# Kernel optimization log

Hardware: AMD Instinct MI355X
Metric: run time of the kernel (lower is better)

Reference implementation:

```python
import jax, jax.numpy as jnp
import numpy as np

HIDDEN = 768
HEAD = 64


def setup_inputs() -> dict:
    key = jax.random.key(0)
    ks = jax.random.split(key, 9)
    s = 1.0 / np.sqrt(HIDDEN)
    so = 1.0 / np.sqrt(HEAD)
    return {
        "x": jax.random.normal(ks[0], (4, 4096, HIDDEN), dtype=jnp.float32),
        "Wq": jax.random.uniform(ks[1], (HIDDEN, HEAD), jnp.float32, -s, s),
        "bq": jax.random.uniform(ks[2], (HEAD,), jnp.float32, -s, s),
        "Wk": jax.random.uniform(ks[3], (HIDDEN, HEAD), jnp.float32, -s, s),
        "bk": jax.random.uniform(ks[4], (HEAD,), jnp.float32, -s, s),
        "Wv": jax.random.uniform(ks[5], (HIDDEN, HEAD), jnp.float32, -s, s),
        "bv": jax.random.uniform(ks[6], (HEAD,), jnp.float32, -s, s),
        "Wo": jax.random.uniform(ks[7], (HEAD, HIDDEN), jnp.float32, -so, so),
        "bo": jax.random.uniform(ks[8], (HIDDEN,), jnp.float32, -so, so),
    }


def reference(x, Wq, bq, Wk, bk, Wv, bv, Wo, bo):
    # x: [b, s, h]
    q = jnp.einsum('bsh,hd->bsd', x, Wq) + bq  # [b, s, d]
    k = jnp.einsum('bsh,hd->bsd', x, Wk) + bk
    v = jnp.einsum('bsh,hd->bsd', x, Wv) + bv
    scale = 1.0 / jnp.sqrt(jnp.asarray(HEAD, x.dtype))
    scores = jnp.einsum('bqd,bkd->bqk', q, k) * scale  # [b, s, s]
    A = jax.nn.softmax(scores, axis=-1)
    ctx = jnp.einsum('bqk,bkd->bqd', A, v)  # [b, s, d]
    return jnp.einsum('bsd,dh->bsh', ctx, Wo) + bo
```

## Files before the change

### kernel.cpp

```cpp
#include <hip/hip_runtime.h>
#include <hip/hip_bf16.h>
#include <stdint.h>

#define BB 4
#define SS 4096
#define HH 768
#define DD 64

typedef __attribute__((ext_vector_type(8))) short bf16x8;
typedef __attribute__((ext_vector_type(4))) short bf16x4;
typedef __attribute__((ext_vector_type(4))) float f32x4;
typedef __attribute__((ext_vector_type(2))) float f32x2;
typedef __attribute__((ext_vector_type(16))) float f32x16;
typedef __attribute__((ext_vector_type(4))) uint32_t u32x4;
typedef __attribute__((ext_vector_type(2))) uint32_t u32x2;

typedef const __attribute__((address_space(1))) uint32_t g_u32;
typedef __attribute__((address_space(3))) uint32_t l_u32;
#define ASYNC16(gp, lp) \
  __builtin_amdgcn_global_load_lds((g_u32*)(gp), (l_u32*)(lp), 16, 0, 0)

__device__ __forceinline__ short f2bf(float f) {
  uint32_t u = __builtin_bit_cast(uint32_t, f);
  u += 0x7fffu + ((u >> 16) & 1u);
  return (short)(u >> 16);
}

#define QSCALE 0.18033688011112042f

__global__ __launch_bounds__(256) void prep_kernel(
    const float* __restrict__ Wq, const float* __restrict__ bq,
    const float* __restrict__ Wk, const float* __restrict__ bk,
    const float* __restrict__ Wv, const float* __restrict__ bv,
    const float* __restrict__ Wo,
    short* __restrict__ wqkvF, float* __restrict__ bqkv,
    short* __restrict__ woF) {
  int idx = blockIdx.x * 256 + threadIdx.x;
  const int N1 = 192 * HH;
  const int N2 = HH * DD;
  if (idx < N1) {
    int n = idx / HH, k = idx % HH;
    float v;
    if (n < 64)       v = Wq[k * 64 + n] * QSCALE;
    else if (n < 128) v = Wk[k * 64 + (n - 64)];
    else              v = Wv[k * 64 + (n - 128)];
    int tile = (n >> 4) * 24 + (k >> 5);
    int lane = (((k >> 3) & 3) << 4) | (n & 15);
    wqkvF[tile * 512 + lane * 8 + (k & 7)] = f2bf(v);
  } else if (idx < N1 + N2) {
    int j = idx - N1;
    int n = j / 64, k = j % 64;
    int tile = (n >> 4) * 2 + (k >> 5);
    int lane = (((k >> 3) & 3) << 4) | (n & 15);
    woF[tile * 512 + lane * 8 + (k & 7)] = f2bf(Wo[k * HH + n]);
  } else if (idx < N1 + N2 + 192) {
    int n = idx - N1 - N2;
    float v;
    if (n < 64)       v = bq[n] * QSCALE;
    else if (n < 128) v = bk[n - 64];
    else              v = bv[n - 128];
    bqkv[n] = v;
  }
}

__global__ __launch_bounds__(256, 2) void qkv_kernel(
    const float* __restrict__ x, const short* __restrict__ wF,
    const float* __restrict__ bqkv,
    short* __restrict__ qb, short* __restrict__ kb, short* __restrict__ vT) {
  __shared__ short xl[32 * 776];
  __shared__ short vtile[64 * 32];
  const int tid = threadIdx.x;
  const int w = tid >> 6, lane = tid & 63, g = (lane >> 4) & 3, n16 = lane & 15;
  const int m0 = blockIdx.x * 32;

  const float4* xsrc = (const float4*)&x[m0 * HH];
#pragma unroll
  for (int i = 0; i < 24; ++i) {
    int idx = i * 256 + tid;
    const float4 f = xsrc[idx];
    int elem = idx * 4;
    int row = elem / HH, col = elem % HH;
    bf16x4 p = { f2bf(f.x), f2bf(f.y), f2bf(f.z), f2bf(f.w) };
    *(bf16x4*)&xl[row * 776 + col] = p;
  }
  __syncthreads();

  f32x4 acc[2][3] = {};
  const short* wbase = &wF[w * 36864 + lane * 8];

#pragma unroll 2
  for (int kc = 0; kc < 24; ++kc) {
    const int ko = kc * 32 + g * 8;
    bf16x8 a0 = *(const bf16x8*)&xl[n16 * 776 + ko];
    bf16x8 a1 = *(const bf16x8*)&xl[(16 + n16) * 776 + ko];
    bf16x8 b0 = *(const bf16x8*)&wbase[kc * 512];
    bf16x8 b1 = *(const bf16x8*)&wbase[12288 + kc * 512];
    bf16x8 b2 = *(const bf16x8*)&wbase[24576 + kc * 512];
    acc[0][0] = __builtin_amdgcn_mfma_f32_16x16x32_bf16(a0, b0, acc[0][0], 0, 0, 0);
    acc[1][0] = __builtin_amdgcn_mfma_f32_16x16x32_bf16(a1, b0, acc[1][0], 0, 0, 0);
    acc[0][1] = __builtin_amdgcn_mfma_f32_16x16x32_bf16(a0, b1, acc[0][1], 0, 0, 0);
    acc[1][1] = __builtin_amdgcn_mfma_f32_16x16x32_bf16(a1, b1, acc[1][1], 0, 0, 0);
    acc[0][2] = __builtin_amdgcn_mfma_f32_16x16x32_bf16(a0, b2, acc[0][2], 0, 0, 0);
    acc[1][2] = __builtin_amdgcn_mfma_f32_16x16x32_bf16(a1, b2, acc[1][2], 0, 0, 0);
  }

#pragma unroll
  for (int ct = 0; ct < 3; ++ct) {
    int nG = w * 48 + ct * 16 + n16;
    float bias = bqkv[nG];
    if (nG < 128) {
#pragma unroll
      for (int rt = 0; rt < 2; ++rt)
#pragma unroll
        for (int r = 0; r < 4; ++r) {
          int rowg = m0 + rt * 16 + g * 4 + r;
          short val = f2bf(acc[rt][ct][r] + bias);
          if (nG < 64) qb[rowg * 64 + nG] = val;
          else         kb[rowg * 64 + (nG - 64)] = val;
        }
    } else {
      int d = nG - 128;
#pragma unroll
      for (int rt = 0; rt < 2; ++rt) {
        bf16x4 p = { f2bf(acc[rt][ct][0] + bias), f2bf(acc[rt][ct][1] + bias),
                     f2bf(acc[rt][ct][2] + bias), f2bf(acc[rt][ct][3] + bias) };
        *(bf16x4*)&vtile[d * 32 + rt * 16 + g * 4] = p;
      }
    }
  }

  __syncthreads();
  {
    int d = tid >> 2, part = tid & 3;
    bf16x8 o = *(const bf16x8*)&vtile[d * 32 + part * 8];
    int b = m0 >> 12;
    *(bf16x8*)&vT[(b * 64 + d) * SS + (m0 & 4095) + part * 8] = o;
  }
}

__global__ __launch_bounds__(256, 4) void flash_kernel(
    const short* __restrict__ qb, const short* __restrict__ kb,
    const short* __restrict__ vT,
    float* __restrict__ Opart, float* __restrict__ lpart) {
  __shared__ short Kl[128 * 64];
  __shared__ short Vl[64 * 128];
  __shared__ float l_lds[64];
  const int tid = threadIdx.x;
  const int w = tid >> 6, lane = tid & 63;
  const int m31 = lane & 31, h = lane >> 5;
  const int qt32 = w & 1, kh = w >> 1;
  const int part = blockIdx.x, rg = part >> 2, sp = part & 3;
  const int b = rg >> 6, qt = rg & 63;
  const short* qB = qb + (b * SS + qt * 64 + qt32 * 32) * DD;
  const short* kB = kb + (b * SS + sp * 1024) * DD;
  const short* vB = vT + b * DD * SS + sp * 1024;

  int srcK[4], srcV[4];
#pragma unroll
  for (int i = 0; i < 4; ++i) {
    int rowK = (w * 4 + i) * 8 + (lane >> 3);
    srcK[i] = rowK * 64 + (((lane & 7) ^ (rowK & 7)) << 3);
    int dV = (w * 4 + i) * 4 + (lane >> 4);
    srcV[i] = dV * SS + (((lane & 15) ^ (dV & 15)) << 3);
  }

  bf16x8 aQ[4];
#pragma unroll
  for (int kk = 0; kk < 4; ++kk)
    aQ[kk] = *(const bf16x8*)&qB[m31 * DD + kk * 16 + 8 * h];

  f32x16 oacc[2] = {};
  float l_run = 0.f;

  for (int kt = 0; kt < 8; ++kt) {
    __syncthreads();
#pragma unroll
    for (int i = 0; i < 4; ++i) {
      ASYNC16(kB + kt * 8192 + srcK[i], &Kl[(w * 4 + i) * 512]);
      ASYNC16(vB + kt * 128  + srcV[i], &Vl[(w * 4 + i) * 512]);
    }
    __syncthreads();

#pragma unroll
    for (int kt2 = 0; kt2 < 2; ++kt2) {
      f32x16 sc = {};
      const int r = kh * 64 + kt2 * 32 + m31;
      const int rx = r & 7;
      __builtin_amdgcn_s_setprio(1);
#pragma unroll
      for (int kk = 0; kk < 4; ++kk) {
        bf16x8 aK = *(const bf16x8*)&Kl[r * 64 + ((((kk << 1) | h) ^ rx) << 3)];
        sc = __builtin_amdgcn_mfma_f32_32x32x16_bf16(aK, aQ[kk], sc, 0, 0, 0);
      }
      __builtin_amdgcn_s_setprio(0);

      f32x2 ls2 = {0.f, 0.f};
      uint32_t pp[8];
#pragma unroll
      for (int j = 0; j < 8; ++j) {
        uint32_t ea = __builtin_bit_cast(uint32_t,
                        __builtin_amdgcn_exp2f(sc[2 * j]));
        uint32_t eb = __builtin_bit_cast(uint32_t,
                        __builtin_amdgcn_exp2f(sc[2 * j + 1]));
        f32x2 t = { __builtin_bit_cast(float, ea & 0xffff0000u),
                    __builtin_bit_cast(float, eb & 0xffff0000u) };
        ls2 += t;
        pp[j] = __builtin_amdgcn_perm(eb, ea, 0x07060302u);
      }
      l_run += ls2.x + ls2.y;

      u32x2 r02 = __builtin_amdgcn_permlane32_swap(pp[0], pp[2], false, false);
      u32x2 r13 = __builtin_amdgcn_permlane32_swap(pp[1], pp[3], false, false);
      u32x2 r46 = __builtin_amdgcn_permlane32_swap(pp[4], pp[6], false, false);
      u32x2 r57 = __builtin_amdgcn_permlane32_swap(pp[5], pp[7], false, false);

#pragma unroll
      for (int s = 0; s < 2; ++s) {
        u32x4 fr = (s == 0) ? u32x4{r02.x, r13.x, r02.y, r13.y}
                            : u32x4{r46.x, r57.x, r46.y, r57.y};
        bf16x8 aP = __builtin_bit_cast(bf16x8, fr);
        const int cv = (kh << 3) | (kt2 << 2) | (s << 1) | h;
        __builtin_amdgcn_s_setprio(1);
#pragma unroll
        for (int dt = 0; dt < 2; ++dt) {
          const int rv = dt * 32 + m31;
          bf16x8 bV = *(const bf16x8*)&Vl[rv * 128 + ((cv ^ (rv & 15)) << 3)];
          oacc[dt] = __builtin_amdgcn_mfma_f32_32x32x16_bf16(aP, bV, oacc[dt], 0, 0, 0);
        }
        __builtin_amdgcn_s_setprio(0);
      }
    }
  }

  l_run += __shfl_xor(l_run, 32);

  __syncthreads();
  float* sO = (float*)Kl;
  if (kh == 1) {
#pragma unroll
    for (int dt = 0; dt < 2; ++dt)
#pragma unroll
      for (int r = 0; r < 16; ++r) {
        int q = (r & 3) + 8 * (r >> 2) + 4 * h;
        sO[qt32 * 2048 + q * 64 + dt * 32 + m31] = oacc[dt][r];
      }
    if (lane < 32) l_lds[qt32 * 32 + lane] = l_run;
  }
  __syncthreads();
  if (kh == 0) {
#pragma unroll
    for (int dt = 0; dt < 2; ++dt)
#pragma unroll
      for (int r = 0; r < 16; ++r) {
        int q = (r & 3) + 8 * (r >> 2) + 4 * h;
        float o = oacc[dt][r] + sO[qt32 * 2048 + q * 64 + dt * 32 + m31];
        Opart[(part * 64 + qt32 * 32 + q) * 64 + dt * 32 + m31] = o;
      }
    if (lane < 32)
      lpart[part * 64 + qt32 * 32 + lane] = l_run + l_lds[qt32 * 32 + lane];
  }
}

__global__ __launch_bounds__(256, 4) void proj_kernel(
    const float* __restrict__ Opart, const float* __restrict__ lpart,
    const short* __restrict__ woF, const float* __restrict__ bo,
    float* __restrict__ out) {
  const int tid = threadIdx.x;
  const int w = tid >> 6, lane = tid & 63, g = lane >> 4, n16 = lane & 15;
  const int m0 = blockIdx.x * 16;
  const int colbase = w * 192;

  const int row = m0 + n16;
  const int rg = row >> 6, r64 = row & 63;
  float lsum = lpart[(rg * 4 + 0) * 64 + r64] + lpart[(rg * 4 + 1) * 64 + r64] +
               lpart[(rg * 4 + 2) * 64 + r64] + lpart[(rg * 4 + 3) * 64 + r64];
  float inv = 1.f / lsum;

  bf16x8 aC[2];
#pragma unroll
  for (int kk = 0; kk < 2; ++kk) {
    const int d0 = kk * 32 + g * 8;
    float s0 = 0, s1 = 0, s2 = 0, s3 = 0, s4 = 0, s5 = 0, s6 = 0, s7 = 0;
#pragma unroll
    for (int sp = 0; sp < 4; ++sp) {
      const float* op = &Opart[((rg * 4 + sp) * 64 + r64) * 64 + d0];
      const float4 v0 = *(const float4*)&op[0];
      const float4 v1 = *(const float4*)&op[4];
      s0 += v0.x; s1 += v0.y; s2 += v0.z; s3 += v0.w;
      s4 += v1.x; s5 += v1.y; s6 += v1.z; s7 += v1.w;
    }
    aC[kk] = bf16x8{ f2bf(s0 * inv), f2bf(s1 * inv), f2bf(s2 * inv), f2bf(s3 * inv),
                     f2bf(s4 * inv), f2bf(s5 * inv), f2bf(s6 * inv), f2bf(s7 * inv) };
  }

  const short* wbase = &woF[w * 12288 + lane * 8];

  f32x4 acc[12] = {};
#pragma unroll
  for (int kk = 0; kk < 2; ++kk) {
#pragma unroll
    for (int ct = 0; ct < 12; ++ct) {
      bf16x8 bW = *(const bf16x8*)&wbase[(ct * 2 + kk) * 512];
      acc[ct] = __builtin_amdgcn_mfma_f32_16x16x32_bf16(aC[kk], bW, acc[ct], 0, 0, 0);
    }
  }
#pragma unroll
  for (int ct = 0; ct < 12; ++ct) {
    int nG = colbase + ct * 16 + n16;
    float bias = bo[nG];
#pragma unroll
    for (int r = 0; r < 4; ++r) {
      int rowg = m0 + g * 4 + r;
      out[rowg * HH + nG] = acc[ct][r] + bias;
    }
  }
}

extern "C" void kernel_launch(void* const* d_in, const int* in_sizes, int n_in,
                              void* d_out, int out_size, void* d_ws, size_t ws_size,
                              hipStream_t stream) {
  const float* x  = (const float*)d_in[0];
  const float* Wq = (const float*)d_in[1];
  const float* bq = (const float*)d_in[2];
  const float* Wk = (const float*)d_in[3];
  const float* bk = (const float*)d_in[4];
  const float* Wv = (const float*)d_in[5];
  const float* bv = (const float*)d_in[6];
  const float* Wo = (const float*)d_in[7];
  const float* bo = (const float*)d_in[8];
  float* out = (float*)d_out;

  char* ws = (char*)d_ws;
  short* qb    = (short*)(ws + 0);
  short* kb    = (short*)(ws + (2u << 20));
  short* vT    = (short*)(ws + (4u << 20));
  short* wqkvF = (short*)(ws + (6u << 20));
  short* woF   = (short*)(ws + (6u << 20) + 384 * 1024);
  float* bqkv  = (float*)(ws + (6u << 20) + 512 * 1024);
  float* lpart = (float*)(ws + (7u << 20));
  float* Opart = (float*)(ws + (8u << 20));

  hipLaunchKernelGGL(prep_kernel, dim3(769), dim3(256), 0, stream,
                     Wq, bq, Wk, bk, Wv, bv, Wo, wqkvF, bqkv, woF);
  hipLaunchKernelGGL(qkv_kernel, dim3(512), dim3(256), 0, stream,
                     x, wqkvF, bqkv, qb, kb, vT);
  hipLaunchKernelGGL(flash_kernel, dim3(1024), dim3(256), 0, stream,
                     qb, kb, vT, Opart, lpart);
  hipLaunchKernelGGL(proj_kernel, dim3(1024), dim3(256), 0, stream,
                     Opart, lpart, woF, bo, out);
}
```

Measured before the change: 159.1 us.

## Double-buffer K/V tiles in flash kernel and halve the key split count

Result: no change. 158.9 us (median of 2 runs) (-0.1%).

```diff
diff --git a/kernel.cpp b/kernel.cpp
--- a/kernel.cpp
+++ b/kernel.cpp
@@ -138,22 +138,22 @@
   }
 }
 
-__global__ __launch_bounds__(256, 4) void flash_kernel(
+__global__ __launch_bounds__(256, 2) void flash_kernel(
     const short* __restrict__ qb, const short* __restrict__ kb,
     const short* __restrict__ vT,
     float* __restrict__ Opart, float* __restrict__ lpart) {
-  __shared__ short Kl[128 * 64];
-  __shared__ short Vl[64 * 128];
+  __shared__ short Kl[2][128 * 64];
+  __shared__ short Vl[2][64 * 128];
   __shared__ float l_lds[64];
   const int tid = threadIdx.x;
   const int w = tid >> 6, lane = tid & 63;
   const int m31 = lane & 31, h = lane >> 5;
   const int qt32 = w & 1, kh = w >> 1;
-  const int part = blockIdx.x, rg = part >> 2, sp = part & 3;
+  const int part = blockIdx.x, rg = part >> 1, sp = part & 1;
   const int b = rg >> 6, qt = rg & 63;
   const short* qB = qb + (b * SS + qt * 64 + qt32 * 32) * DD;
-  const short* kB = kb + (b * SS + sp * 1024) * DD;
-  const short* vB = vT + b * DD * SS + sp * 1024;
+  const short* kB = kb + (b * SS + sp * 2048) * DD;
+  const short* vB = vT + b * DD * SS + sp * 2048;
 
   int srcK[4], srcV[4];
 #pragma unroll
@@ -172,14 +172,28 @@
   f32x16 oacc[2] = {};
   float l_run = 0.f;
 
-  for (int kt = 0; kt < 8; ++kt) {
-    __syncthreads();
-#pragma unroll
-    for (int i = 0; i < 4; ++i) {
-      ASYNC16(kB + kt * 8192 + srcK[i], &Kl[(w * 4 + i) * 512]);
-      ASYNC16(vB + kt * 128  + srcV[i], &Vl[(w * 4 + i) * 512]);
-    }
-    __syncthreads();
+#pragma unroll
+  for (int i = 0; i < 4; ++i) {
+    ASYNC16(kB + srcK[i], &Kl[0][(w * 4 + i) * 512]);
+    ASYNC16(vB + srcV[i], &Vl[0][(w * 4 + i) * 512]);
+  }
+
+  for (int kt = 0; kt < 16; ++kt) {
+    const int cur = kt & 1;
+    if (kt < 15) {
+      const short* kN = kB + (kt + 1) * 8192;
+      const short* vN = vB + (kt + 1) * 128;
+#pragma unroll
+      for (int i = 0; i < 4; ++i) {
+        ASYNC16(kN + srcK[i], &Kl[cur ^ 1][(w * 4 + i) * 512]);
+        ASYNC16(vN + srcV[i], &Vl[cur ^ 1][(w * 4 + i) * 512]);
+      }
+      asm volatile("s_waitcnt vmcnt(8)" ::: "memory");
+    } else {
+      asm volatile("s_waitcnt vmcnt(0)" ::: "memory");
+    }
+    __builtin_amdgcn_s_barrier();
+    __builtin_amdgcn_sched_barrier(0);
 
 #pragma unroll
     for (int kt2 = 0; kt2 < 2; ++kt2) {
@@ -189,7 +203,7 @@
       __builtin_amdgcn_s_setprio(1);
 #pragma unroll
       for (int kk = 0; kk < 4; ++kk) {
-        bf16x8 aK = *(const bf16x8*)&Kl[r * 64 + ((((kk << 1) | h) ^ rx) << 3)];
+        bf16x8 aK = *(const bf16x8*)&Kl[cur][r * 64 + ((((kk << 1) | h) ^ rx) << 3)];
         sc = __builtin_amdgcn_mfma_f32_32x32x16_bf16(aK, aQ[kk], sc, 0, 0, 0);
       }
       __builtin_amdgcn_s_setprio(0);
@@ -224,18 +238,20 @@
 #pragma unroll
         for (int dt = 0; dt < 2; ++dt) {
           const int rv = dt * 32 + m31;
-          bf16x8 bV = *(const bf16x8*)&Vl[rv * 128 + ((cv ^ (rv & 15)) << 3)];
+          bf16x8 bV = *(const bf16x8*)&Vl[cur][rv * 128 + ((cv ^ (rv & 15)) << 3)];
           oacc[dt] = __builtin_amdgcn_mfma_f32_32x32x16_bf16(aP, bV, oacc[dt], 0, 0, 0);
         }
         __builtin_amdgcn_s_setprio(0);
       }
     }
+    __builtin_amdgcn_sched_barrier(0);
+    __builtin_amdgcn_s_barrier();
   }
 
   l_run += __shfl_xor(l_run, 32);
 
   __syncthreads();
-  float* sO = (float*)Kl;
+  float* sO = (float*)&Kl[0][0];
   if (kh == 1) {
 #pragma unroll
     for (int dt = 0; dt < 2; ++dt)
@@ -272,8 +288,7 @@
 
   const int row = m0 + n16;
   const int rg = row >> 6, r64 = row & 63;
-  float lsum = lpart[(rg * 4 + 0) * 64 + r64] + lpart[(rg * 4 + 1) * 64 + r64] +
-               lpart[(rg * 4 + 2) * 64 + r64] + lpart[(rg * 4 + 3) * 64 + r64];
+  float lsum = lpart[(rg * 2 + 0) * 64 + r64] + lpart[(rg * 2 + 1) * 64 + r64];
   float inv = 1.f / lsum;
 
   bf16x8 aC[2];
@@ -282,8 +297,8 @@
     const int d0 = kk * 32 + g * 8;
     float s0 = 0, s1 = 0, s2 = 0, s3 = 0, s4 = 0, s5 = 0, s6 = 0, s7 = 0;
 #pragma unroll
-    for (int sp = 0; sp < 4; ++sp) {
-      const float* op = &Opart[((rg * 4 + sp) * 64 + r64) * 64 + d0];
+    for (int sp = 0; sp < 2; ++sp) {
+      const float* op = &Opart[((rg * 2 + sp) * 64 + r64) * 64 + d0];
       const float4 v0 = *(const float4*)&op[0];
       const float4 v1 = *(const float4*)&op[4];
       s0 += v0.x; s1 += v0.y; s2 += v0.z; s3 += v0.w;
@@ -344,7 +359,7 @@
                      Wq, bq, Wk, bk, Wv, bv, Wo, wqkvF, bqkv, woF);
   hipLaunchKernelGGL(qkv_kernel, dim3(512), dim3(256), 0, stream,
                      x, wqkvF, bqkv, qb, kb, vT);
-  hipLaunchKernelGGL(flash_kernel, dim3(1024), dim3(256), 0, stream,
+  hipLaunchKernelGGL(flash_kernel, dim3(512), dim3(256), 0, stream,
                      qb, kb, vT, Opart, lpart);
   hipLaunchKernelGGL(proj_kernel, dim3(1024), dim3(256), 0, stream,
                      Opart, lpart, woF, bo, out);
```

## Load K directly to registers and double-buffer V tiles in LDS

Applied to the files above, without the earlier changes.

Result: slower. 172.7 us (+8.6%).

```diff
diff --git a/kernel.cpp b/kernel.cpp
--- a/kernel.cpp
+++ b/kernel.cpp
@@ -142,8 +142,7 @@
     const short* __restrict__ qb, const short* __restrict__ kb,
     const short* __restrict__ vT,
     float* __restrict__ Opart, float* __restrict__ lpart) {
-  __shared__ short Kl[128 * 64];
-  __shared__ short Vl[64 * 128];
+  __shared__ short Vl[2][8192];
   __shared__ float l_lds[64];
   const int tid = threadIdx.x;
   const int w = tid >> 6, lane = tid & 63;
@@ -155,14 +154,13 @@
   const short* kB = kb + (b * SS + sp * 1024) * DD;
   const short* vB = vT + b * DD * SS + sp * 1024;
 
-  int srcK[4], srcV[4];
+  int srcV[4];
 #pragma unroll
   for (int i = 0; i < 4; ++i) {
-    int rowK = (w * 4 + i) * 8 + (lane >> 3);
-    srcK[i] = rowK * 64 + (((lane & 7) ^ (rowK & 7)) << 3);
     int dV = (w * 4 + i) * 4 + (lane >> 4);
     srcV[i] = dV * SS + (((lane & 15) ^ (dV & 15)) << 3);
   }
+  const short* kRow = kB + (kh * 64 + m31) * DD + 8 * h;
 
   bf16x8 aQ[4];
 #pragma unroll
@@ -172,26 +170,38 @@
   f32x16 oacc[2] = {};
   float l_run = 0.f;
 
+#pragma unroll
+  for (int i = 0; i < 4; ++i)
+    ASYNC16(vB + srcV[i], &Vl[0][(w * 4 + i) * 512]);
+
   for (int kt = 0; kt < 8; ++kt) {
-    __syncthreads();
-#pragma unroll
-    for (int i = 0; i < 4; ++i) {
-      ASYNC16(kB + kt * 8192 + srcK[i], &Kl[(w * 4 + i) * 512]);
-      ASYNC16(vB + kt * 128  + srcV[i], &Vl[(w * 4 + i) * 512]);
-    }
-    __syncthreads();
+    const int cur = kt & 1;
+    __builtin_amdgcn_s_barrier();
+    if (kt < 7) {
+      const short* vN = vB + (kt + 1) * 128;
+#pragma unroll
+      for (int i = 0; i < 4; ++i)
+        ASYNC16(vN + srcV[i], &Vl[cur ^ 1][(w * 4 + i) * 512]);
+      asm volatile("s_waitcnt vmcnt(4)" ::: "memory");
+    } else {
+      asm volatile("s_waitcnt vmcnt(0)" ::: "memory");
+    }
+    __builtin_amdgcn_s_barrier();
+    __builtin_amdgcn_sched_barrier(0);
 
 #pragma unroll
     for (int kt2 = 0; kt2 < 2; ++kt2) {
+      const short* kP = kRow + kt * 8192 + kt2 * 2048;
+      bf16x8 aK[4];
+#pragma unroll
+      for (int kk = 0; kk < 4; ++kk)
+        aK[kk] = *(const bf16x8*)&kP[kk * 16];
+
       f32x16 sc = {};
-      const int r = kh * 64 + kt2 * 32 + m31;
-      const int rx = r & 7;
       __builtin_amdgcn_s_setprio(1);
 #pragma unroll
-      for (int kk = 0; kk < 4; ++kk) {
-        bf16x8 aK = *(const bf16x8*)&Kl[r * 64 + ((((kk << 1) | h) ^ rx) << 3)];
-        sc = __builtin_amdgcn_mfma_f32_32x32x16_bf16(aK, aQ[kk], sc, 0, 0, 0);
-      }
+      for (int kk = 0; kk < 4; ++kk)
+        sc = __builtin_amdgcn_mfma_f32_32x32x16_bf16(aK[kk], aQ[kk], sc, 0, 0, 0);
       __builtin_amdgcn_s_setprio(0);
 
       f32x2 ls2 = {0.f, 0.f};
@@ -224,18 +234,19 @@
 #pragma unroll
         for (int dt = 0; dt < 2; ++dt) {
           const int rv = dt * 32 + m31;
-          bf16x8 bV = *(const bf16x8*)&Vl[rv * 128 + ((cv ^ (rv & 15)) << 3)];
+          bf16x8 bV = *(const bf16x8*)&Vl[cur][rv * 128 + ((cv ^ (rv & 15)) << 3)];
           oacc[dt] = __builtin_amdgcn_mfma_f32_32x32x16_bf16(aP, bV, oacc[dt], 0, 0, 0);
         }
         __builtin_amdgcn_s_setprio(0);
       }
     }
+    __builtin_amdgcn_sched_barrier(0);
   }
 
   l_run += __shfl_xor(l_run, 32);
 
   __syncthreads();
-  float* sO = (float*)Kl;
+  float* sO = (float*)&Vl[0][0];
   if (kh == 1) {
 #pragma unroll
     for (int dt = 0; dt < 2; ++dt)
```

## Double-buffer K/V tiles in flash kernel with async prefetch of next tile

Applied to the files above, without the earlier changes.

Result: no change. 160.8 us (+1.1%).

```diff
diff --git a/kernel.cpp b/kernel.cpp
--- a/kernel.cpp
+++ b/kernel.cpp
@@ -142,8 +142,8 @@
     const short* __restrict__ qb, const short* __restrict__ kb,
     const short* __restrict__ vT,
     float* __restrict__ Opart, float* __restrict__ lpart) {
-  __shared__ short Kl[128 * 64];
-  __shared__ short Vl[64 * 128];
+  __shared__ short Kl[2][64 * 64];
+  __shared__ short Vl[2][64 * 64];
   __shared__ float l_lds[64];
   const int tid = threadIdx.x;
   const int w = tid >> 6, lane = tid & 63;
@@ -155,13 +155,13 @@
   const short* kB = kb + (b * SS + sp * 1024) * DD;
   const short* vB = vT + b * DD * SS + sp * 1024;
 
-  int srcK[4], srcV[4];
-#pragma unroll
-  for (int i = 0; i < 4; ++i) {
-    int rowK = (w * 4 + i) * 8 + (lane >> 3);
+  int srcK[2], srcV[2];
+#pragma unroll
+  for (int i = 0; i < 2; ++i) {
+    int rowK = (w * 2 + i) * 8 + (lane >> 3);
     srcK[i] = rowK * 64 + (((lane & 7) ^ (rowK & 7)) << 3);
-    int dV = (w * 4 + i) * 4 + (lane >> 4);
-    srcV[i] = dV * SS + (((lane & 15) ^ (dV & 15)) << 3);
+    int dV = (w * 2 + i) * 8 + (lane >> 3);
+    srcV[i] = dV * SS + (((lane & 7) ^ (dV & 7)) << 3);
   }
 
   bf16x8 aQ[4];
@@ -172,24 +172,37 @@
   f32x16 oacc[2] = {};
   float l_run = 0.f;
 
-  for (int kt = 0; kt < 8; ++kt) {
-    __syncthreads();
-#pragma unroll
-    for (int i = 0; i < 4; ++i) {
-      ASYNC16(kB + kt * 8192 + srcK[i], &Kl[(w * 4 + i) * 512]);
-      ASYNC16(vB + kt * 128  + srcV[i], &Vl[(w * 4 + i) * 512]);
-    }
-    __syncthreads();
-
-#pragma unroll
-    for (int kt2 = 0; kt2 < 2; ++kt2) {
+#pragma unroll
+  for (int i = 0; i < 2; ++i) {
+    ASYNC16(kB + srcK[i], &Kl[0][(w * 2 + i) * 512]);
+    ASYNC16(vB + srcV[i], &Vl[0][(w * 2 + i) * 512]);
+  }
+
+  for (int kt = 0; kt < 16; ++kt) {
+    const int cur = kt & 1;
+    if (kt < 15) {
+      const short* kN = kB + (kt + 1) * 4096;
+      const short* vN = vB + (kt + 1) * 64;
+#pragma unroll
+      for (int i = 0; i < 2; ++i) {
+        ASYNC16(kN + srcK[i], &Kl[cur ^ 1][(w * 2 + i) * 512]);
+        ASYNC16(vN + srcV[i], &Vl[cur ^ 1][(w * 2 + i) * 512]);
+      }
+      asm volatile("s_waitcnt vmcnt(4)" ::: "memory");
+    } else {
+      asm volatile("s_waitcnt vmcnt(0)" ::: "memory");
+    }
+    __builtin_amdgcn_s_barrier();
+    __builtin_amdgcn_sched_barrier(0);
+
+    {
       f32x16 sc = {};
-      const int r = kh * 64 + kt2 * 32 + m31;
+      const int r = kh * 32 + m31;
       const int rx = r & 7;
       __builtin_amdgcn_s_setprio(1);
 #pragma unroll
       for (int kk = 0; kk < 4; ++kk) {
-        bf16x8 aK = *(const bf16x8*)&Kl[r * 64 + ((((kk << 1) | h) ^ rx) << 3)];
+        bf16x8 aK = *(const bf16x8*)&Kl[cur][r * 64 + ((((kk << 1) | h) ^ rx) << 3)];
         sc = __builtin_amdgcn_mfma_f32_32x32x16_bf16(aK, aQ[kk], sc, 0, 0, 0);
       }
       __builtin_amdgcn_s_setprio(0);
@@ -219,23 +232,25 @@
         u32x4 fr = (s == 0) ? u32x4{r02.x, r13.x, r02.y, r13.y}
                             : u32x4{r46.x, r57.x, r46.y, r57.y};
         bf16x8 aP = __builtin_bit_cast(bf16x8, fr);
-        const int cv = (kh << 3) | (kt2 << 2) | (s << 1) | h;
+        const int cv = (kh << 2) | (s << 1) | h;
         __builtin_amdgcn_s_setprio(1);
 #pragma unroll
         for (int dt = 0; dt < 2; ++dt) {
           const int rv = dt * 32 + m31;
-          bf16x8 bV = *(const bf16x8*)&Vl[rv * 128 + ((cv ^ (rv & 15)) << 3)];
+          bf16x8 bV = *(const bf16x8*)&Vl[cur][rv * 64 + ((cv ^ (rv & 7)) << 3)];
           oacc[dt] = __builtin_amdgcn_mfma_f32_32x32x16_bf16(aP, bV, oacc[dt], 0, 0, 0);
         }
         __builtin_amdgcn_s_setprio(0);
       }
     }
+    __builtin_amdgcn_sched_barrier(0);
+    __builtin_amdgcn_s_barrier();
   }
 
   l_run += __shfl_xor(l_run, 32);
 
   __syncthreads();
-  float* sO = (float*)Kl;
+  float* sO = (float*)&Kl[0][0];
   if (kh == 1) {
 #pragma unroll
     for (int dt = 0; dt < 2; ++dt)
```
